# Performance work log

Measured on AMD Instinct MI355X. Metric: run time of the kernel, lower is better.

The kernel has to match this reference:

```python
import jax, jax.numpy as jnp
import numpy as np

N, D, H, G = 262144, 256, 8, 2048
DH = D // H  # 32


def setup_inputs() -> dict:
    key = jax.random.key(0)
    ks = jax.random.split(key, 12)
    s = 0.02
    x = jax.random.normal(ks[0], (N, D), jnp.float32)
    # equal-size sets: batch[i] = set id, ptr = CSR boundaries (consistent pair)
    batch = jnp.repeat(jnp.arange(G, dtype=jnp.int64), N // G)
    ptr = jnp.arange(G + 1, dtype=jnp.int64) * (N // G)
    rn = lambda k, sh: jax.random.normal(k, sh, jnp.float32) * s
    return {
        "x": x, "ptr": ptr, "batch": batch,
        "lin_w": rn(ks[1], (D, D)), "lin_b": jnp.zeros((D,), jnp.float32),
        "seed": rn(ks[2], (D,)),
        "wq": rn(ks[3], (D, D)), "bq": jnp.zeros((D,), jnp.float32),
        "wk": rn(ks[4], (D, D)), "bk": jnp.zeros((D,), jnp.float32),
        "wv": rn(ks[5], (D, D)), "bv": jnp.zeros((D,), jnp.float32),
        "wo": rn(ks[6], (D, D)), "bo": jnp.zeros((D,), jnp.float32),
        "mlp_w1": rn(ks[7], (D, D)), "mlp_b1": jnp.zeros((D,), jnp.float32),
        "mlp_w2": rn(ks[8], (D, D)), "mlp_b2": jnp.zeros((D,), jnp.float32),
    }


def gelu(v):
    return jax.nn.gelu(v, approximate=False)  # torch nn.GELU default (erf)


def reference(x, ptr, batch, lin_w, lin_b, seed, wq, bq, wk, bk, wv, bv,
              wo, bo, mlp_w1, mlp_b1, mlp_w2, mlp_b2):
    # pre-projection + GELU
    h = gelu(x @ lin_w + lin_b)                         # [N, D]
    # PMA-style multihead attention pooling over ragged sets
    q = (seed @ wq + bq).reshape(H, DH)                 # learnable seed query per head
    k = (h @ wk + bk).reshape(-1, H, DH)                # [N, H, DH]
    v = (h @ wv + bv).reshape(-1, H, DH)                # [N, H, DH]
    scores = jnp.einsum('nhd,hd->nh', k, q) / jnp.sqrt(jnp.float32(DH))  # [N, H]
    # segment (per-set) numerically-stable softmax
    m = jax.ops.segment_max(scores, batch, num_segments=G)   # [G, H]
    e = jnp.exp(scores - m[batch])
    z = jax.ops.segment_sum(e, batch, num_segments=G)        # [G, H]
    w = e / z[batch]                                         # [N, H] attention weights
    pooled = jax.ops.segment_sum(w[:, :, None] * v, batch, num_segments=G)  # [G, H, DH]
    pooled = pooled.reshape(G, D) @ wo + bo                  # output projection [G, D]
    # 2-layer MLP head (plain_last: no act on final layer; dropout=0 at eval)
    out = gelu(pooled @ mlp_w1 + mlp_b1) @ mlp_w2 + mlp_b2   # [G, D]
    return out
```

## Files before the change

kernel.cpp:

```cpp
#include <hip/hip_runtime.h>
#include <hip/hip_bf16.h>

#define DD 256
#define SETSZ 128
#define NSETS 2048

typedef __attribute__((ext_vector_type(8))) __bf16 bf16x8;
typedef __attribute__((ext_vector_type(8))) unsigned short u16x8;
typedef __attribute__((ext_vector_type(4))) float f32x4;

static __device__ __forceinline__ unsigned short f2bf(float f) {
    unsigned u = __builtin_bit_cast(unsigned, f);
    u += 0x7fffu + ((u >> 16) & 1u);
    return (unsigned short)(u >> 16);
}

static __device__ __forceinline__ float gelu_f(float v) {
    return 0.5f * v * (1.0f + erff(v * 0.70710678118654752f));
}

__global__ void prep1_kernel(const float* __restrict__ seed, const float* __restrict__ wq,
                             const float* __restrict__ bq, float* __restrict__ q) {
    int j = threadIdx.x;
    float s = bq[j];
#pragma unroll 16
    for (int d = 0; d < DD; ++d) s += seed[d] * wq[d * DD + j];
    q[j] = s;
}

__global__ void prep2_kernel(const float* __restrict__ lin_w, const float* __restrict__ wv,
                             const float* __restrict__ wk, const float* __restrict__ q,
                             unsigned short* __restrict__ linT, unsigned short* __restrict__ wvT,
                             unsigned short* __restrict__ wkqB) {
    int b = blockIdx.x, t = threadIdx.x;
    if (b < DD) {
        linT[b * DD + t] = f2bf(lin_w[t * DD + b]);
        wvT[b * DD + t]  = f2bf(wv[t * DD + b]);
    } else {
        const float inv = 0.17677669529663687f;
        for (int c = 0; c < 8; ++c) {
            float s = 0.f;
#pragma unroll 8
            for (int j = 0; j < 32; ++j) s += wk[t * DD + c * 32 + j] * q[c * 32 + j];
            wkqB[c * DD + t] = f2bf(s * inv);
        }
        for (int c = 8; c < 16; ++c) wkqB[c * DD + t] = 0;
    }
}

__global__ __launch_bounds__(512, 2)
void attn_pool_kernel(const float* __restrict__ x, const float* __restrict__ lin_b,
                      const float* __restrict__ bv,
                      const unsigned short* __restrict__ linT,
                      const unsigned short* __restrict__ wvT,
                      const unsigned short* __restrict__ wkqB,
                      float* __restrict__ pooled) {
    __shared__ unsigned short xs[SETSZ * DD];
    const int g = blockIdx.x;
    const int t = threadIdx.x;
    const int lane = t & 63;
    const int wid = t >> 6;
    const int l15 = lane & 15;
    const int kg = lane >> 4;
    const long r0 = (long)g * SETSZ;

#pragma unroll
    for (int i = 0; i < 8; ++i) {
        int c = i * 512 + t;
        int row = c >> 5;
        int cg = c & 31;
        const float4* src = reinterpret_cast<const float4*>(x + (r0 + row) * DD + cg * 8);
        float4 a0 = src[0];
        float4 a1 = src[1];
        u16x8 v;
        v[0] = f2bf(a0.x); v[1] = f2bf(a0.y); v[2] = f2bf(a0.z); v[3] = f2bf(a0.w);
        v[4] = f2bf(a1.x); v[5] = f2bf(a1.y); v[6] = f2bf(a1.z); v[7] = f2bf(a1.w);
        int sg = cg ^ (row & 7);
        *reinterpret_cast<u16x8*>(&xs[row * DD + sg * 8]) = v;
    }
    __syncthreads();

    const int colbase = wid * 32;

    f32x4 acc[8][2];
#pragma unroll
    for (int r = 0; r < 8; ++r) { acc[r][0] = 0.f; acc[r][1] = 0.f; }

#pragma unroll
    for (int ks = 0; ks < 8; ++ks) {
        bf16x8 af[8];
#pragma unroll
        for (int r = 0; r < 8; ++r) {
            int row = r * 16 + l15;
            int sg = (ks * 4 + kg) ^ (row & 7);
            af[r] = *reinterpret_cast<const bf16x8*>(&xs[row * DD + sg * 8]);
        }
        int bofs = ks * 32 + kg * 8;
        bf16x8 b0 = *reinterpret_cast<const bf16x8*>(linT + (colbase + l15) * DD + bofs);
        bf16x8 b1 = *reinterpret_cast<const bf16x8*>(linT + (colbase + 16 + l15) * DD + bofs);
#pragma unroll
        for (int r = 0; r < 8; ++r) {
            acc[r][0] = __builtin_amdgcn_mfma_f32_16x16x32_bf16(af[r], b0, acc[r][0], 0, 0, 0);
            acc[r][1] = __builtin_amdgcn_mfma_f32_16x16x32_bf16(af[r], b1, acc[r][1], 0, 0, 0);
        }
    }
    __syncthreads();

    {
        float lb0 = lin_b[colbase + l15];
        float lb1 = lin_b[colbase + 16 + l15];
#pragma unroll
        for (int r = 0; r < 8; ++r) {
#pragma unroll
            for (int c = 0; c < 2; ++c) {
                int col = colbase + c * 16 + l15;
                float lb = c ? lb1 : lb0;
#pragma unroll
                for (int j = 0; j < 4; ++j) {
                    int row = r * 16 + kg * 4 + j;
                    float hv = gelu_f(acc[r][c][j] + lb);
                    int sg = (col >> 3) ^ (row & 7);
                    xs[row * DD + sg * 8 + (col & 7)] = f2bf(hv);
                }
            }
        }
    }
    __syncthreads();

    f32x4 vacc[8][2];
    f32x4 sacc[8];
#pragma unroll
    for (int r = 0; r < 8; ++r) { vacc[r][0] = 0.f; vacc[r][1] = 0.f; sacc[r] = 0.f; }

#pragma unroll
    for (int ks = 0; ks < 8; ++ks) {
        bf16x8 af[8];
#pragma unroll
        for (int r = 0; r < 8; ++r) {
            int row = r * 16 + l15;
            int sg = (ks * 4 + kg) ^ (row & 7);
            af[r] = *reinterpret_cast<const bf16x8*>(&xs[row * DD + sg * 8]);
        }
        int bofs = ks * 32 + kg * 8;
        bf16x8 b0 = *reinterpret_cast<const bf16x8*>(wvT + (colbase + l15) * DD + bofs);
        bf16x8 b1 = *reinterpret_cast<const bf16x8*>(wvT + (colbase + 16 + l15) * DD + bofs);
        bf16x8 bq8 = *reinterpret_cast<const bf16x8*>(wkqB + l15 * DD + bofs);
#pragma unroll
        for (int r = 0; r < 8; ++r) {
            vacc[r][0] = __builtin_amdgcn_mfma_f32_16x16x32_bf16(af[r], b0, vacc[r][0], 0, 0, 0);
            vacc[r][1] = __builtin_amdgcn_mfma_f32_16x16x32_bf16(af[r], b1, vacc[r][1], 0, 0, 0);
            sacc[r]    = __builtin_amdgcn_mfma_f32_16x16x32_bf16(af[r], bq8, sacc[r], 0, 0, 0);
        }
    }

    float e[8][4];
    float mx = -1e30f;
#pragma unroll
    for (int r = 0; r < 8; ++r)
#pragma unroll
        for (int j = 0; j < 4; ++j) {
            float s = __shfl(sacc[r][j], (lane & 48) | wid, 64);
            e[r][j] = s;
            mx = fmaxf(mx, s);
        }
    mx = fmaxf(mx, __shfl_xor(mx, 16, 64));
    mx = fmaxf(mx, __shfl_xor(mx, 32, 64));
    float z = 0.f;
#pragma unroll
    for (int r = 0; r < 8; ++r)
#pragma unroll
        for (int j = 0; j < 4; ++j) {
            float ee = __expf(e[r][j] - mx);
            e[r][j] = ee;
            z += ee;
        }
    z += __shfl_xor(z, 16, 64);
    z += __shfl_xor(z, 32, 64);
    float inv = 1.0f / z;

#pragma unroll
    for (int c = 0; c < 2; ++c) {
        float pp = 0.f;
#pragma unroll
        for (int r = 0; r < 8; ++r)
#pragma unroll
            for (int j = 0; j < 4; ++j) pp += e[r][j] * vacc[r][c][j];
        pp *= inv;
        pp += __shfl_xor(pp, 16, 64);
        pp += __shfl_xor(pp, 32, 64);
        if (kg == 0) {
            int col = colbase + c * 16 + l15;
            pooled[(long)g * DD + col] = pp + bv[col];
        }
    }
}

__global__ __launch_bounds__(256)
void mlp_kernel(const float* __restrict__ pooled,
                const float* __restrict__ wo, const float* __restrict__ bo,
                const float* __restrict__ w1, const float* __restrict__ b1,
                const float* __restrict__ w2, const float* __restrict__ b2,
                float* __restrict__ out) {
    __shared__ float sa[8][DD];
    __shared__ float sb[8][DD];
    const int c = threadIdx.x;
    const long base = (long)blockIdx.x * 8 * DD;
#pragma unroll
    for (int r = 0; r < 8; ++r) sa[r][c] = pooled[base + r * DD + c];
    __syncthreads();
    {
        float acc[8];
        float bb = bo[c];
#pragma unroll
        for (int r = 0; r < 8; ++r) acc[r] = bb;
#pragma unroll 4
        for (int k = 0; k < DD; ++k) {
            float wvv = wo[k * DD + c];
#pragma unroll
            for (int r = 0; r < 8; ++r) acc[r] += sa[r][k] * wvv;
        }
#pragma unroll
        for (int r = 0; r < 8; ++r) sb[r][c] = acc[r];
    }
    __syncthreads();
    {
        float acc[8];
        float bb = b1[c];
#pragma unroll
        for (int r = 0; r < 8; ++r) acc[r] = bb;
#pragma unroll 4
        for (int k = 0; k < DD; ++k) {
            float wvv = w1[k * DD + c];
#pragma unroll
            for (int r = 0; r < 8; ++r) acc[r] += sb[r][k] * wvv;
        }
#pragma unroll
        for (int r = 0; r < 8; ++r) sa[r][c] = gelu_f(acc[r]);
    }
    __syncthreads();
    {
        float acc[8];
        float bb = b2[c];
#pragma unroll
        for (int r = 0; r < 8; ++r) acc[r] = bb;
#pragma unroll 4
        for (int k = 0; k < DD; ++k) {
            float wvv = w2[k * DD + c];
#pragma unroll
            for (int r = 0; r < 8; ++r) acc[r] += sa[r][k] * wvv;
        }
#pragma unroll
        for (int r = 0; r < 8; ++r) out[base + r * DD + c] = acc[r];
    }
}

extern "C" void kernel_launch(void* const* d_in, const int* in_sizes, int n_in,
                              void* d_out, int out_size, void* d_ws, size_t ws_size,
                              hipStream_t stream) {
    const float* x     = (const float*)d_in[0];
    const float* lin_w = (const float*)d_in[3];
    const float* lin_b = (const float*)d_in[4];
    const float* seed  = (const float*)d_in[5];
    const float* wq    = (const float*)d_in[6];
    const float* bq    = (const float*)d_in[7];
    const float* wk    = (const float*)d_in[8];
    const float* wvp   = (const float*)d_in[10];
    const float* bv    = (const float*)d_in[11];
    const float* wo    = (const float*)d_in[12];
    const float* bo    = (const float*)d_in[13];
    const float* w1    = (const float*)d_in[14];
    const float* b1    = (const float*)d_in[15];
    const float* w2    = (const float*)d_in[16];
    const float* b2    = (const float*)d_in[17];
    float* out = (float*)d_out;

    char* ws = (char*)d_ws;
    float* q             = (float*)ws;
    unsigned short* wkqB = (unsigned short*)(ws + 4096);
    unsigned short* linT = (unsigned short*)(ws + 16384);
    unsigned short* wvT  = (unsigned short*)(ws + 16384 + 131072);
    float* pooled        = (float*)(ws + 16384 + 262144);

    prep1_kernel<<<1, 256, 0, stream>>>(seed, wq, bq, q);
    prep2_kernel<<<257, 256, 0, stream>>>(lin_w, wvp, wk, q, linT, wvT, wkqB);
    attn_pool_kernel<<<NSETS, 512, 0, stream>>>(x, lin_b, bv, linT, wvT, wkqB, pooled);
    mlp_kernel<<<NSETS / 8, 256, 0, stream>>>(pooled, wo, bo, w1, b1, w2, b2, out);
}
```

Measured before the change: 250.7 us.

## Retile attention-pool kernel into 2x4 warp grid with split score/softmax phases

Restructures the fused attention-pool kernel so each warp computes a 64-row by 64-column tile (2 row halves x 4 column quarters) with weights as the MFMA A operand, raising register-level reuse and reducing per-warp LDS reads. Scores are computed once by one warp per row half, with the softmax max and sum exchanged through shared-memory buffers, and the weighted V reduction uses a butterfly shuffle transpose. It also replaces erff with an Abramowitz-Stegun polynomial GELU using a fast reciprocal, adds an extra XOR term to the LDS swizzle, uses lgkmcnt-only barriers, and raises launch bounds to 4 blocks. In exchange it adds more barriers and LDS traffic for cross-warp softmax, idles three warps per half during the score phase, and uses a less accurate erf.

```diff
diff --git a/kernel.cpp b/kernel.cpp
--- a/kernel.cpp
+++ b/kernel.cpp
@@ -16,8 +16,26 @@
 }
 
 static __device__ __forceinline__ float gelu_f(float v) {
-    return 0.5f * v * (1.0f + erff(v * 0.70710678118654752f));
-}
+    float ax = fabsf(v) * 0.70710678118654752f;
+    float t = __builtin_amdgcn_rcpf(__builtin_fmaf(0.3275911f, ax, 1.0f));
+    float p = __builtin_fmaf(1.061405429f, t, -1.453152027f);
+    p = __builtin_fmaf(p, t, 1.421413741f);
+    p = __builtin_fmaf(p, t, -0.284496736f);
+    p = __builtin_fmaf(p, t, 0.254829592f);
+    p = p * t;
+    float er = __builtin_fmaf(-p, __expf(-ax * ax), 1.0f);
+    er = copysignf(er, v);
+    return 0.5f * v * (1.0f + er);
+}
+
+static __device__ __forceinline__ int swz(int row, int cg) {
+    return cg ^ (row & 7) ^ ((row >> 3) & 3);
+}
+
+#define LGKM_BARRIER() do { \
+    asm volatile("s_waitcnt lgkmcnt(0)" ::: "memory"); \
+    __builtin_amdgcn_s_barrier(); \
+} while (0)
 
 __global__ void prep1_kernel(const float* __restrict__ seed, const float* __restrict__ wq,
                              const float* __restrict__ bq, float* __restrict__ q) {
@@ -48,7 +66,7 @@
     }
 }
 
-__global__ __launch_bounds__(512, 2)
+__global__ __launch_bounds__(512, 4)
 void attn_pool_kernel(const float* __restrict__ x, const float* __restrict__ lin_b,
                       const float* __restrict__ bv,
                       const unsigned short* __restrict__ linT,
@@ -56,142 +74,242 @@
                       const unsigned short* __restrict__ wkqB,
                       float* __restrict__ pooled) {
     __shared__ unsigned short xs[SETSZ * DD];
+    __shared__ float wbuf[SETSZ][8];
+    __shared__ float mzbuf[2][16];
+    __shared__ float zbuf[2][16];
+    __shared__ float pbuf[2][DD];
+
     const int g = blockIdx.x;
     const int t = threadIdx.x;
     const int lane = t & 63;
     const int wid = t >> 6;
+    const int rh = wid >> 2;
+    const int cq = wid & 3;
     const int l15 = lane & 15;
     const int kg = lane >> 4;
+    const int colq = cq * 64;
+    const int rowbase = rh * 64;
     const long r0 = (long)g * SETSZ;
 
-#pragma unroll
-    for (int i = 0; i < 8; ++i) {
-        int c = i * 512 + t;
-        int row = c >> 5;
-        int cg = c & 31;
-        const float4* src = reinterpret_cast<const float4*>(x + (r0 + row) * DD + cg * 8);
-        float4 a0 = src[0];
-        float4 a1 = src[1];
-        u16x8 v;
-        v[0] = f2bf(a0.x); v[1] = f2bf(a0.y); v[2] = f2bf(a0.z); v[3] = f2bf(a0.w);
-        v[4] = f2bf(a1.x); v[5] = f2bf(a1.y); v[6] = f2bf(a1.z); v[7] = f2bf(a1.w);
-        int sg = cg ^ (row & 7);
-        *reinterpret_cast<u16x8*>(&xs[row * DD + sg * 8]) = v;
-    }
-    __syncthreads();
-
-    const int colbase = wid * 32;
-
-    f32x4 acc[8][2];
-#pragma unroll
-    for (int r = 0; r < 8; ++r) { acc[r][0] = 0.f; acc[r][1] = 0.f; }
+    {
+        const float* bx = x + r0 * DD;
+#pragma unroll
+        for (int half = 0; half < 2; ++half) {
+            float4 L[8];
+#pragma unroll
+            for (int qq = 0; qq < 4; ++qq) {
+                int c = (half * 4 + qq) * 512 + t;
+                const float4* src = reinterpret_cast<const float4*>(bx + (c >> 5) * DD + (c & 31) * 8);
+                L[2 * qq] = src[0];
+                L[2 * qq + 1] = src[1];
+            }
+#pragma unroll
+            for (int qq = 0; qq < 4; ++qq) {
+                int c = (half * 4 + qq) * 512 + t;
+                int row = c >> 5, cg = c & 31;
+                u16x8 v;
+                v[0] = f2bf(L[2*qq].x);   v[1] = f2bf(L[2*qq].y);
+                v[2] = f2bf(L[2*qq].z);   v[3] = f2bf(L[2*qq].w);
+                v[4] = f2bf(L[2*qq+1].x); v[5] = f2bf(L[2*qq+1].y);
+                v[6] = f2bf(L[2*qq+1].z); v[7] = f2bf(L[2*qq+1].w);
+                *reinterpret_cast<u16x8*>(&xs[row * DD + swz(row, cg) * 8]) = v;
+            }
+        }
+    }
+    LGKM_BARRIER();
+
+    f32x4 acc[4][4];
+#pragma unroll
+    for (int ab = 0; ab < 4; ++ab)
+#pragma unroll
+        for (int nb = 0; nb < 4; ++nb) acc[ab][nb] = 0.f;
 
 #pragma unroll
     for (int ks = 0; ks < 8; ++ks) {
-        bf16x8 af[8];
-#pragma unroll
-        for (int r = 0; r < 8; ++r) {
-            int row = r * 16 + l15;
-            int sg = (ks * 4 + kg) ^ (row & 7);
-            af[r] = *reinterpret_cast<const bf16x8*>(&xs[row * DD + sg * 8]);
-        }
-        int bofs = ks * 32 + kg * 8;
-        bf16x8 b0 = *reinterpret_cast<const bf16x8*>(linT + (colbase + l15) * DD + bofs);
-        bf16x8 b1 = *reinterpret_cast<const bf16x8*>(linT + (colbase + 16 + l15) * DD + bofs);
-#pragma unroll
-        for (int r = 0; r < 8; ++r) {
-            acc[r][0] = __builtin_amdgcn_mfma_f32_16x16x32_bf16(af[r], b0, acc[r][0], 0, 0, 0);
-            acc[r][1] = __builtin_amdgcn_mfma_f32_16x16x32_bf16(af[r], b1, acc[r][1], 0, 0, 0);
-        }
-    }
-    __syncthreads();
-
-    {
-        float lb0 = lin_b[colbase + l15];
-        float lb1 = lin_b[colbase + 16 + l15];
-#pragma unroll
-        for (int r = 0; r < 8; ++r) {
-#pragma unroll
-            for (int c = 0; c < 2; ++c) {
-                int col = colbase + c * 16 + l15;
-                float lb = c ? lb1 : lb0;
-#pragma unroll
-                for (int j = 0; j < 4; ++j) {
-                    int row = r * 16 + kg * 4 + j;
-                    float hv = gelu_f(acc[r][c][j] + lb);
-                    int sg = (col >> 3) ^ (row & 7);
-                    xs[row * DD + sg * 8 + (col & 7)] = f2bf(hv);
-                }
-            }
-        }
-    }
-    __syncthreads();
-
-    f32x4 vacc[8][2];
-    f32x4 sacc[8];
-#pragma unroll
-    for (int r = 0; r < 8; ++r) { vacc[r][0] = 0.f; vacc[r][1] = 0.f; sacc[r] = 0.f; }
-
+        bf16x8 A[4], B[4];
+#pragma unroll
+        for (int ab = 0; ab < 4; ++ab)
+            A[ab] = *reinterpret_cast<const bf16x8*>(linT + (colq + 16 * ab + l15) * DD + ks * 32 + kg * 8);
+#pragma unroll
+        for (int nb = 0; nb < 4; ++nb) {
+            int row = rowbase + 16 * nb + l15;
+            B[nb] = *reinterpret_cast<const bf16x8*>(&xs[row * DD + swz(row, ks * 4 + kg) * 8]);
+        }
+#pragma unroll
+        for (int ab = 0; ab < 4; ++ab)
+#pragma unroll
+            for (int nb = 0; nb < 4; ++nb)
+                acc[ab][nb] = __builtin_amdgcn_mfma_f32_16x16x32_bf16(A[ab], B[nb], acc[ab][nb], 0, 0, 0);
+    }
+    LGKM_BARRIER();
+
+    {
+#pragma unroll
+        for (int ab = 0; ab < 4; ++ab) {
+            const float4 lb4 = *reinterpret_cast<const float4*>(lin_b + colq + 16 * ab + 4 * kg);
+            int cg = (colq >> 3) + 2 * ab + (kg >> 1);
+#pragma unroll
+            for (int nb = 0; nb < 4; ++nb) {
+                int row = rowbase + 16 * nb + l15;
+                float g0 = gelu_f(acc[ab][nb][0] + lb4.x);
+                float g1 = gelu_f(acc[ab][nb][1] + lb4.y);
+                float g2 = gelu_f(acc[ab][nb][2] + lb4.z);
+                float g3 = gelu_f(acc[ab][nb][3] + lb4.w);
+                unsigned d0 = (unsigned)f2bf(g0) | ((unsigned)f2bf(g1) << 16);
+                unsigned d1 = (unsigned)f2bf(g2) | ((unsigned)f2bf(g3) << 16);
+                *reinterpret_cast<uint2*>(&xs[row * DD + swz(row, cg) * 8 + (kg & 1) * 4]) =
+                    make_uint2(d0, d1);
+            }
+        }
+    }
+    LGKM_BARRIER();
+
+    f32x4 sacc[4];
+    sacc[0] = 0.f; sacc[1] = 0.f; sacc[2] = 0.f; sacc[3] = 0.f;
+    if (cq == 0) {
+#pragma unroll
+        for (int ks = 0; ks < 8; ++ks) {
+            bf16x8 Aq = *reinterpret_cast<const bf16x8*>(wkqB + l15 * DD + ks * 32 + kg * 8);
+#pragma unroll
+            for (int nb = 0; nb < 4; ++nb) {
+                int row = rowbase + 16 * nb + l15;
+                bf16x8 B = *reinterpret_cast<const bf16x8*>(&xs[row * DD + swz(row, ks * 4 + kg) * 8]);
+                sacc[nb] = __builtin_amdgcn_mfma_f32_16x16x32_bf16(Aq, B, sacc[nb], 0, 0, 0);
+            }
+        }
+        float mj[4];
+#pragma unroll
+        for (int j = 0; j < 4; ++j)
+            mj[j] = fmaxf(fmaxf(sacc[0][j], sacc[1][j]), fmaxf(sacc[2][j], sacc[3][j]));
+#pragma unroll
+        for (int st = 1; st < 16; st <<= 1)
+#pragma unroll
+            for (int j = 0; j < 4; ++j) mj[j] = fmaxf(mj[j], __shfl_xor(mj[j], st, 64));
+        if (l15 == 0) {
+            f32x4 mv; mv[0] = mj[0]; mv[1] = mj[1]; mv[2] = mj[2]; mv[3] = mj[3];
+            *reinterpret_cast<f32x4*>(&mzbuf[rh][4 * kg]) = mv;
+        }
+    }
+    LGKM_BARRIER();
+
+    if (cq == 0) {
+        f32x4 m0 = *reinterpret_cast<const f32x4*>(&mzbuf[0][4 * kg]);
+        f32x4 m1 = *reinterpret_cast<const f32x4*>(&mzbuf[1][4 * kg]);
+        float mf[4], zj[4];
+#pragma unroll
+        for (int j = 0; j < 4; ++j) { mf[j] = fmaxf(m0[j], m1[j]); zj[j] = 0.f; }
+        f32x4 e4[4];
+#pragma unroll
+        for (int nb = 0; nb < 4; ++nb)
+#pragma unroll
+            for (int j = 0; j < 4; ++j) {
+                float e = __expf(sacc[nb][j] - mf[j]);
+                e4[nb][j] = e;
+                zj[j] += e;
+            }
+#pragma unroll
+        for (int st = 1; st < 16; st <<= 1)
+#pragma unroll
+            for (int j = 0; j < 4; ++j) zj[j] += __shfl_xor(zj[j], st, 64);
+        if (l15 == 0) {
+            f32x4 zv; zv[0] = zj[0]; zv[1] = zj[1]; zv[2] = zj[2]; zv[3] = zj[3];
+            *reinterpret_cast<f32x4*>(&zbuf[rh][4 * kg]) = zv;
+        }
+        if (kg < 2) {
+#pragma unroll
+            for (int nb = 0; nb < 4; ++nb) {
+                int row = rowbase + 16 * nb + l15;
+                *reinterpret_cast<f32x4*>(&wbuf[row][4 * kg]) = e4[nb];
+            }
+        }
+    }
+    LGKM_BARRIER();
+
+    f32x4 vacc[4][4];
+#pragma unroll
+    for (int ab = 0; ab < 4; ++ab)
+#pragma unroll
+        for (int nb = 0; nb < 4; ++nb) vacc[ab][nb] = 0.f;
 #pragma unroll
     for (int ks = 0; ks < 8; ++ks) {
-        bf16x8 af[8];
-#pragma unroll
-        for (int r = 0; r < 8; ++r) {
-            int row = r * 16 + l15;
-            int sg = (ks * 4 + kg) ^ (row & 7);
-            af[r] = *reinterpret_cast<const bf16x8*>(&xs[row * DD + sg * 8]);
-        }
-        int bofs = ks * 32 + kg * 8;
-        bf16x8 b0 = *reinterpret_cast<const bf16x8*>(wvT + (colbase + l15) * DD + bofs);
-        bf16x8 b1 = *reinterpret_cast<const bf16x8*>(wvT + (colbase + 16 + l15) * DD + bofs);
-        bf16x8 bq8 = *reinterpret_cast<const bf16x8*>(wkqB + l15 * DD + bofs);
-#pragma unroll
-        for (int r = 0; r < 8; ++r) {
-            vacc[r][0] = __builtin_amdgcn_mfma_f32_16x16x32_bf16(af[r], b0, vacc[r][0], 0, 0, 0);
-            vacc[r][1] = __builtin_amdgcn_mfma_f32_16x16x32_bf16(af[r], b1, vacc[r][1], 0, 0, 0);
-            sacc[r]    = __builtin_amdgcn_mfma_f32_16x16x32_bf16(af[r], bq8, sacc[r], 0, 0, 0);
-        }
-    }
-
-    float e[8][4];
-    float mx = -1e30f;
-#pragma unroll
-    for (int r = 0; r < 8; ++r)
-#pragma unroll
-        for (int j = 0; j < 4; ++j) {
-            float s = __shfl(sacc[r][j], (lane & 48) | wid, 64);
-            e[r][j] = s;
-            mx = fmaxf(mx, s);
-        }
-    mx = fmaxf(mx, __shfl_xor(mx, 16, 64));
-    mx = fmaxf(mx, __shfl_xor(mx, 32, 64));
-    float z = 0.f;
-#pragma unroll
-    for (int r = 0; r < 8; ++r)
-#pragma unroll
-        for (int j = 0; j < 4; ++j) {
-            float ee = __expf(e[r][j] - mx);
-            e[r][j] = ee;
-            z += ee;
-        }
-    z += __shfl_xor(z, 16, 64);
-    z += __shfl_xor(z, 32, 64);
-    float inv = 1.0f / z;
-
-#pragma unroll
-    for (int c = 0; c < 2; ++c) {
-        float pp = 0.f;
-#pragma unroll
-        for (int r = 0; r < 8; ++r)
-#pragma unroll
-            for (int j = 0; j < 4; ++j) pp += e[r][j] * vacc[r][c][j];
-        pp *= inv;
-        pp += __shfl_xor(pp, 16, 64);
-        pp += __shfl_xor(pp, 32, 64);
-        if (kg == 0) {
-            int col = colbase + c * 16 + l15;
-            pooled[(long)g * DD + col] = pp + bv[col];
-        }
+        bf16x8 A[4], B[4];
+#pragma unroll
+        for (int ab = 0; ab < 4; ++ab)
+            A[ab] = *reinterpret_cast<const bf16x8*>(wvT + (colq + 16 * ab + l15) * DD + ks * 32 + kg * 8);
+#pragma unroll
+        for (int nb = 0; nb < 4; ++nb) {
+            int row = rowbase + 16 * nb + l15;
+            B[nb] = *reinterpret_cast<const bf16x8*>(&xs[row * DD + swz(row, ks * 4 + kg) * 8]);
+        }
+#pragma unroll
+        for (int ab = 0; ab < 4; ++ab)
+#pragma unroll
+            for (int nb = 0; nb < 4; ++nb)
+                vacc[ab][nb] = __builtin_amdgcn_mfma_f32_16x16x32_bf16(A[ab], B[nb], vacc[ab][nb], 0, 0, 0);
+    }
+
+    {
+        float w0[4], w1[4];
+#pragma unroll
+        for (int nb = 0; nb < 4; ++nb) {
+            int row = rowbase + 16 * nb + l15;
+            w0[nb] = wbuf[row][2 * cq];
+            w1[nb] = wbuf[row][2 * cq + 1];
+        }
+        float v16[16];
+#pragma unroll
+        for (int ab = 0; ab < 4; ++ab)
+#pragma unroll
+            for (int j = 0; j < 4; ++j) {
+                float s = 0.f;
+#pragma unroll
+                for (int nb = 0; nb < 4; ++nb)
+                    s += (ab < 2 ? w0[nb] : w1[nb]) * vacc[ab][nb][j];
+                v16[ab * 4 + j] = s;
+            }
+        float v8[8], v4[4], v2[2], vf;
+        {
+            bool b = (l15 & 1);
+#pragma unroll
+            for (int i = 0; i < 8; ++i) {
+                float keep = b ? v16[2 * i + 1] : v16[2 * i];
+                float send = b ? v16[2 * i] : v16[2 * i + 1];
+                v8[i] = keep + __shfl_xor(send, 1, 64);
+            }
+        }
+        {
+            bool b = (l15 >> 1) & 1;
+#pragma unroll
+            for (int i = 0; i < 4; ++i) {
+                float keep = b ? v8[2 * i + 1] : v8[2 * i];
+                float send = b ? v8[2 * i] : v8[2 * i + 1];
+                v4[i] = keep + __shfl_xor(send, 2, 64);
+            }
+        }
+        {
+            bool b = (l15 >> 2) & 1;
+#pragma unroll
+            for (int i = 0; i < 2; ++i) {
+                float keep = b ? v4[2 * i + 1] : v4[2 * i];
+                float send = b ? v4[2 * i] : v4[2 * i + 1];
+                v2[i] = keep + __shfl_xor(send, 4, 64);
+            }
+        }
+        {
+            bool b = (l15 >> 3) & 1;
+            float keep = b ? v2[1] : v2[0];
+            float send = b ? v2[0] : v2[1];
+            vf = keep + __shfl_xor(send, 8, 64);
+        }
+        int vcol = colq + 16 * (l15 >> 2) + 4 * kg + (l15 & 3);
+        pbuf[rh][vcol] = vf;
+    }
+    LGKM_BARRIER();
+
+    if (t < DD) {
+        int hh = t >> 5;
+        float z = zbuf[0][hh] + zbuf[1][hh];
+        pooled[(long)g * DD + t] = (pbuf[0][t] + pbuf[1][t]) / z + bv[t];
     }
 }
 
```

Measured after the change: 311.1 us. 1.24x slower.
